# Optimization experiments

Measured on AMD Instinct MI355X. Metric: run time of the kernel, lower is better.

The kernel has to match this reference:

```python
import jax, jax.numpy as jnp
import numpy as np

NUM_HEADS = 8
POS_DIM = 4
LEFT_CTX = 512


def setup_inputs() -> dict:
    key = jax.random.key(0)
    ks = jax.random.split(key, 9)
    S, B, E, A, H, P, L = 512, 16, 512, 512, NUM_HEADS, POS_DIM, LEFT_CTX
    in_out = 2 * A + A // 2 + H * P  # 1312
    S2 = 2 * S - 1 + L  # 1535
    return {
        "x": jax.random.normal(ks[0], (S, B, E), jnp.float32) * 0.1,
        "cached_key": jax.random.normal(ks[1], (L, B, A), jnp.float32) * 0.1,
        "cached_val": jax.random.normal(ks[2], (L, B, A // 2), jnp.float32) * 0.1,
        "pos_emb": jax.random.normal(ks[3], (1, S2, E), jnp.float32) * 0.1,
        "in_proj_w": jax.random.normal(ks[4], (in_out, E), jnp.float32) * 0.02,
        "in_proj_b": jnp.zeros((in_out,), jnp.float32),
        "linear_pos_w": jax.random.normal(ks[5], (H * P, E), jnp.float32) * 0.02,
        "out_proj_w": jax.random.normal(ks[6], (E, A // 2), jnp.float32) * 0.02,
        "out_proj_b": jnp.zeros((E,), jnp.float32),
    }


def reference(x, cached_key, cached_val, pos_emb, in_proj_w, in_proj_b,
              linear_pos_w, out_proj_w, out_proj_b):
    S, B, E = x.shape
    L = cached_key.shape[0]
    A = cached_key.shape[-1]          # attention_dim
    H, P = NUM_HEADS, POS_DIM
    hd = A // H                        # head_dim
    vd = hd // 2                       # value head dim

    # in_proj (nn.Linear): (S, B, 2A + A/2 + H*P)
    xp = jnp.einsum('sbe,oe->sbo', x, in_proj_w) + in_proj_b
    q = xp[..., :A]
    k_new = xp[..., A:2 * A]
    v_new = xp[..., 2 * A:2 * A + A // 2]
    p = xp[..., 2 * A + A // 2:]

    # pad+add == concat(cached, new) along time
    k = jnp.concatenate([cached_key, k_new], axis=0)   # (kv, B, A)
    v = jnp.concatenate([cached_val, v_new], axis=0)   # (kv, B, A/2)
    cached_key_out = k[-L:]
    cached_val_out = v[-L:]
    kv = k.shape[0]

    q4 = q.reshape(S, B, H, hd)
    p4 = p.reshape(S, B, H, P)
    k4 = k.reshape(kv, B, H, hd)
    v4 = v.reshape(kv, B, H, vd)

    # relative position bias: linear_pos has no bias
    S2 = pos_emb.shape[1]              # 2S - 1 + L
    pos = (jnp.einsum('one,pe->onp', pos_emb, linear_pos_w)
           .reshape(S2, H, P))          # (S2, H, P)
    pos_weights = jnp.einsum('sbhp,nhp->bhsn', p4, pos)  # (B, H, S, S2)

    # as_strided relative shift: out[b,h,t,j] = pw[b,h,t, (S-1) - t + j]
    idx = (S - 1) - jnp.arange(S)[:, None] + jnp.arange(kv)[None, :]  # (S, kv)
    pos_weights = jnp.take_along_axis(pos_weights, idx[None, None], axis=3)

    scores = jnp.einsum('sbhd,nbhd->bhsn', q4, k4) + pos_weights  # (B,H,S,kv)
    attn = jax.nn.softmax(scores, axis=-1)

    out = jnp.einsum('bhsn,nbhd->sbhd', attn, v4).reshape(S, B, A // 2)
    out = jnp.einsum('sbd,ed->sbe', out, out_proj_w) + out_proj_b

    weights = attn.reshape(B * H, S, kv)
    return out, weights, cached_key_out, cached_val_out
```

## Files before the change

### kernel.cpp

```cpp
#include <hip/hip_runtime.h>
#include <math.h>


using f32x4  = __attribute__((ext_vector_type(4))) float;
using bf16x8 = __attribute__((ext_vector_type(8))) short;

__device__ __forceinline__ unsigned short f2bf(float f) {
    unsigned u = __builtin_bit_cast(unsigned, f);
    u = (u + 0x7FFFu + ((u >> 16) & 1u)) >> 16;
    return (unsigned short)u;
}
__device__ __forceinline__ float bf2f(unsigned short s) {
    return __builtin_bit_cast(float, (unsigned)s << 16);
}

__device__ __forceinline__ void cvt8(const float* __restrict__ src,
                                     unsigned short* __restrict__ dst, int i)
{
    float4 v0 = *(const float4*)(src + i);
    float4 v1 = *(const float4*)(src + i + 4);
    unsigned short tmp[8] = { f2bf(v0.x), f2bf(v0.y), f2bf(v0.z), f2bf(v0.w),
                              f2bf(v1.x), f2bf(v1.y), f2bf(v1.z), f2bf(v1.w) };
    *(int4*)(dst + i) = *(const int4*)tmp;
}

__global__ __launch_bounds__(256)
void prep(const float* __restrict__ x, const float* __restrict__ in_proj_w,
          const float* __restrict__ out_proj_w, const float* __restrict__ ck_in,
          const float* __restrict__ pos_emb, const float* __restrict__ lpw,
          unsigned short* __restrict__ xb, unsigned short* __restrict__ wb,
          unsigned short* __restrict__ opw, unsigned short* __restrict__ kb,
          float* __restrict__ pos_ws)
{
    __shared__ float As[16][68];
    __shared__ float Bs[16][68];
    const int bid = blockIdx.x, t = threadIdx.x;
    if (bid < 2048) {
        cvt8(x, xb, (bid * 256 + t) * 8);
    } else if (bid < 2376) {
        cvt8(in_proj_w, wb, ((bid - 2048) * 256 + t) * 8);
    } else if (bid < 2440) {
        cvt8(out_proj_w, opw, ((bid - 2376) * 256 + t) * 8);
    } else if (bid < 3464) {
        const int i  = bid - 2440;
        const int n0 = (i & 63) * 8;
        const int b  = i >> 6;
        const int c  = t * 2;
        const int h  = c >> 6, d = c & 63;
        #pragma unroll
        for (int j = 0; j < 8; ++j) {
            const int n = n0 + j;
            float2 v = *(const float2*)(ck_in + ((size_t)n * 16 + b) * 512 + c);
            unsigned short tmp[2] = { f2bf(v.x), f2bf(v.y) };
            *(unsigned int*)(kb + (((size_t)b*8 + h)*1024 + n)*64 + d)
                = *(const unsigned int*)tmp;
        }
    } else {
        const int m0 = (bid - 3464) * 64;
        const int lr = t >> 2, lc = (t & 3) * 4;
        const int tx = t & 15, ty = t >> 4;
        float acc[4][4] = {};
        for (int k0 = 0; k0 < 512; k0 += 16) {
            float4 av = make_float4(0.f,0.f,0.f,0.f);
            float4 bv = make_float4(0.f,0.f,0.f,0.f);
            if (m0 + lr < 1535) av = *(const float4*)(pos_emb + (size_t)(m0 + lr) * 512 + k0 + lc);
            if (lr < 32)        bv = *(const float4*)(lpw + (size_t)lr * 512 + k0 + lc);
            __syncthreads();
            As[lc+0][lr] = av.x; As[lc+1][lr] = av.y; As[lc+2][lr] = av.z; As[lc+3][lr] = av.w;
            Bs[lc+0][lr] = bv.x; Bs[lc+1][lr] = bv.y; Bs[lc+2][lr] = bv.z; Bs[lc+3][lr] = bv.w;
            __syncthreads();
            #pragma unroll
            for (int kk = 0; kk < 16; ++kk) {
                float4 a4 = *(const float4*)&As[kk][ty * 4];
                float4 b4 = *(const float4*)&Bs[kk][tx * 4];
                float af[4] = {a4.x, a4.y, a4.z, a4.w};
                float bf[4] = {b4.x, b4.y, b4.z, b4.w};
                #pragma unroll
                for (int i2 = 0; i2 < 4; ++i2)
                    #pragma unroll
                    for (int j = 0; j < 4; ++j)
                        acc[i2][j] += af[i2] * bf[j];
            }
        }
        const int n = tx * 4;
        if (n < 32) {
            #pragma unroll
            for (int i2 = 0; i2 < 4; ++i2) {
                const int mi = m0 + ty * 4 + i2;
                if (mi >= 1535) break;
                #pragma unroll
                for (int j = 0; j < 4; ++j)
                    pos_ws[(size_t)mi * 32 + n + j] = acc[i2][j];
            }
        }
    }
}

__global__ __launch_bounds__(256)
void mfma_gemm_nt(const unsigned short* __restrict__ A,
                  const unsigned short* __restrict__ B,
                  const float* __restrict__ bias, int K, int N, int NBLK, int mode,
                  float* __restrict__ C, int ldc,
                  unsigned short* __restrict__ qb, float* __restrict__ ck,
                  unsigned short* __restrict__ kb, float* __restrict__ cv,
                  float* __restrict__ p_ws)
{
    __shared__ unsigned short smem[6144];
    const int t  = threadIdx.x;
    const int wv = t >> 6, l = t & 63;
    const int lr = l & 15, g = l >> 4;
    const int bid = blockIdx.x;
    const int xcd = bid & 7, i = bid >> 3;
    const int my  = xcd + 8 * (i / NBLK);
    const int nx  = i % NBLK;
    const int m0b = my * 128;
    const int m0  = m0b + wv * 32;
    const int n0  = nx * 64;

    const int srow = t >> 2, soct = t & 3;
    const unsigned short* Ag0 = A + (size_t)(m0b + srow) * K + soct * 8;
    const unsigned short* Ag1 = Ag0 + (size_t)64 * K;
    const unsigned short* Bg  = B + (size_t)(n0 + srow) * K + soct * 8;
    const int oa0 = (soct * 128 + srow) * 8;
    const int oa1 = oa0 + 64 * 8;
    const int ob  = 4096 + (soct * 64 + srow) * 8;

    const int ra0 = (g * 128 + wv * 32 + lr) * 8;
    const int ra1 = ra0 + 16 * 8;
    const int rb  = 4096 + (g * 64 + lr) * 8;

    f32x4 acc[2][4] = {};

    bf16x8 sa0 = *(const bf16x8*)(Ag0);
    bf16x8 sa1 = *(const bf16x8*)(Ag1);
    bf16x8 sb  = *(const bf16x8*)(Bg);

    const int NK = K >> 5;
    for (int t16 = 0; t16 < NK; ++t16) {
        __syncthreads();
        *(bf16x8*)(smem + oa0) = sa0;
        *(bf16x8*)(smem + oa1) = sa1;
        *(bf16x8*)(smem + ob)  = sb;
        __syncthreads();
        if (t16 + 1 < NK) {
            const int k0 = (t16 + 1) * 32;
            sa0 = *(const bf16x8*)(Ag0 + k0);
            sa1 = *(const bf16x8*)(Ag1 + k0);
            sb  = *(const bf16x8*)(Bg + k0);
        }
        bf16x8 a0 = *(const bf16x8*)(smem + ra0);
        bf16x8 a1 = *(const bf16x8*)(smem + ra1);
        bf16x8 b0 = *(const bf16x8*)(smem + rb);
        bf16x8 b1 = *(const bf16x8*)(smem + rb + 16 * 8);
        bf16x8 b2 = *(const bf16x8*)(smem + rb + 32 * 8);
        bf16x8 b3 = *(const bf16x8*)(smem + rb + 48 * 8);
        acc[0][0] = __builtin_amdgcn_mfma_f32_16x16x32_bf16(a0, b0, acc[0][0], 0, 0, 0);
        acc[0][1] = __builtin_amdgcn_mfma_f32_16x16x32_bf16(a0, b1, acc[0][1], 0, 0, 0);
        acc[0][2] = __builtin_amdgcn_mfma_f32_16x16x32_bf16(a0, b2, acc[0][2], 0, 0, 0);
        acc[0][3] = __builtin_amdgcn_mfma_f32_16x16x32_bf16(a0, b3, acc[0][3], 0, 0, 0);
        acc[1][0] = __builtin_amdgcn_mfma_f32_16x16x32_bf16(a1, b0, acc[1][0], 0, 0, 0);
        acc[1][1] = __builtin_amdgcn_mfma_f32_16x16x32_bf16(a1, b1, acc[1][1], 0, 0, 0);
        acc[1][2] = __builtin_amdgcn_mfma_f32_16x16x32_bf16(a1, b2, acc[1][2], 0, 0, 0);
        acc[1][3] = __builtin_amdgcn_mfma_f32_16x16x32_bf16(a1, b3, acc[1][3], 0, 0, 0);
    }

    const int rbase = g * 4;
    const int nf = (N - n0) >= 64 ? 4 : (N - n0) >> 4;
    #pragma unroll
    for (int fi = 0; fi < 2; ++fi) {
        for (int fj = 0; fj < nf; ++fj) {
            const f32x4& a = acc[fi][fj];
            const int c = n0 + fj * 16 + lr;
            const float bs = bias ? bias[c] : 0.f;
            #pragma unroll
            for (int r = 0; r < 4; ++r) {
                const int m = m0 + fi * 16 + rbase + r;
                const float v = a[r] + bs;
                if (mode == 0) {
                    C[(size_t)m * ldc + c] = v;
                } else {
                    const int s = m >> 4, bb = m & 15;
                    if (c < 512) {
                        const int hh = c >> 6, dd = c & 63;
                        qb[(((size_t)bb*8 + hh)*512 + s)*64 + dd] = f2bf(v);
                    } else if (c < 1024) {
                        const int cc = c - 512;
                        __builtin_nontemporal_store(v, ck + (size_t)m * 512 + cc);
                        const int hh = cc >> 6, dd = cc & 63;
                        kb[(((size_t)bb*8 + hh)*1024 + 512 + s)*64 + dd] = f2bf(v);
                    } else if (c < 1280) {
                        cv[(size_t)m * 256 + (c - 1024)] = v;
                    } else {
                        p_ws[(size_t)m * 32 + (c - 1280)] = v;
                    }
                }
            }
        }
    }
}

__global__ __launch_bounds__(256)
void transpose_v(const float* __restrict__ cv_in, const float* __restrict__ cv_new,
                 unsigned short* __restrict__ vt)
{
    const int t  = threadIdx.x;
    const int n0 = blockIdx.x * 128;
    const int bh = blockIdx.y;
    const int b  = bh >> 3, h = bh & 7;

    __shared__ float tile[128][33];

    #pragma unroll
    for (int k = 0; k < 4; ++k) {
        const int nl = (t >> 3) + k * 32;
        const int n  = n0 + nl;
        const int c4 = (t & 7) * 4;
        const float* src = (n < 512)
            ? cv_in  + ((size_t)n * 16 + b) * 256 + h * 32 + c4
            : cv_new + ((size_t)(n - 512) * 16 + b) * 256 + h * 32 + c4;
        float4 v = *(const float4*)src;
        tile[nl][c4 + 0] = v.x; tile[nl][c4 + 1] = v.y;
        tile[nl][c4 + 2] = v.z; tile[nl][c4 + 3] = v.w;
    }
    __syncthreads();
    {
        const int d  = t >> 3;
        const int nb = (t & 7) * 16;
        unsigned short tmp[16];
        #pragma unroll
        for (int j = 0; j < 16; ++j) tmp[j] = f2bf(tile[nb + j][d]);
        unsigned short* dst = vt + ((size_t)bh * 32 + d) * 1024 + n0 + nb;
        *(int4*)(dst)     = *(const int4*)(tmp);
        *(int4*)(dst + 8) = *(const int4*)(tmp + 8);
    }
}

__global__ __launch_bounds__(256, 4)
void attn_fused2(const unsigned short* __restrict__ qb,
                 const float* __restrict__ p_ws,
                 const float* __restrict__ pos_ws,
                 const unsigned short* __restrict__ kb,
                 const unsigned short* __restrict__ vt,
                 float* __restrict__ weights,
                 unsigned short* __restrict__ ao)
{
    const int t  = threadIdx.x;
    const int wv = t >> 6, l = t & 63;
    const int lr = l & 15, ks0 = (l >> 4) * 8, rbase = (l >> 4) * 4;
    const int idx = blockIdx.x;
    const int kq  = idx >> 3;
    const int bh  = (idx & 7) + 8 * (kq >> 5);
    const int s0  = (kq & 31) * 16;
    const int b   = bh >> 3, h = bh & 7;

    union SM { float4 pos[1039]; unsigned short e[16][1064]; };
    __shared__ SM u;
    __shared__ float pvred[4][16][16];
    __shared__ float red_l[4][16];

    const int j0 = 496 - s0;
    for (int j = t; j < 1039; j += 256)
        u.pos[j] = *(const float4*)(pos_ws + (size_t)(j0 + j) * 32 + h * 4);

    const unsigned short* qp = qb + ((size_t)bh * 512 + s0 + lr) * 64 + ks0;
    bf16x8 qa0 = *(const bf16x8*)(qp);
    bf16x8 qa1 = *(const bf16x8*)(qp + 32);

    float4 p4r[4];
    #pragma unroll
    for (int r = 0; r < 4; ++r)
        p4r[r] = *(const float4*)(p_ws + ((size_t)(s0 + rbase + r) * 16 + b) * 32 + h * 4);

    const unsigned short* kbase = kb + ((size_t)bh * 1024 + wv * 256) * 64;
    f32x4 sc[16];
    #pragma unroll
    for (int i = 0; i < 16; ++i) sc[i] = (f32x4){0.f,0.f,0.f,0.f};

    #pragma unroll
    for (int tile = 0; tile < 16; ++tile) {
        const unsigned short* kp = kbase + (size_t)(tile * 16 + lr) * 64 + ks0;
        bf16x8 k0 = *(const bf16x8*)(kp);
        bf16x8 k1 = *(const bf16x8*)(kp + 32);
        sc[tile] = __builtin_amdgcn_mfma_f32_16x16x32_bf16(qa0, k0, sc[tile], 0, 0, 0);
        sc[tile] = __builtin_amdgcn_mfma_f32_16x16x32_bf16(qa1, k1, sc[tile], 0, 0, 0);
    }

    __syncthreads();

    float sm[4] = {0.f, 0.f, 0.f, 0.f};
    #pragma unroll
    for (int tile = 0; tile < 16; ++tile) {
        const int nidx = wv * 256 + tile * 16 + lr;
        #pragma unroll
        for (int r = 0; r < 4; ++r) {
            float4 pp = u.pos[15 - rbase - r + nidx];
            float e = __expf(sc[tile][r] + p4r[r].x * pp.x + p4r[r].y * pp.y
                                         + p4r[r].z * pp.z + p4r[r].w * pp.w);
            sc[tile][r] = e;
            sm[r] += e;
        }
    }
    #pragma unroll
    for (int r = 0; r < 4; ++r) {
        #pragma unroll
        for (int off = 1; off < 16; off <<= 1) sm[r] += __shfl_xor(sm[r], off);
    }

    __syncthreads();

    if (lr == 0) {
        #pragma unroll
        for (int r = 0; r < 4; ++r) red_l[wv][rbase + r] = sm[r];
    }
    #pragma unroll
    for (int tile = 0; tile < 16; ++tile) {
        const int nidx = wv * 256 + tile * 16 + lr;
        #pragma unroll
        for (int r = 0; r < 4; ++r)
            u.e[rbase + r][nidx] = f2bf(sc[tile][r]);
    }
    __syncthreads();

    const int kh = wv >> 1, dt = wv & 1;
    f32x4 paA = {0.f, 0.f, 0.f, 0.f}, paB = {0.f, 0.f, 0.f, 0.f};
    const unsigned short* vrow = vt + ((size_t)bh * 32 + dt * 16 + lr) * 1024;
    #pragma unroll
    for (int kstep = 0; kstep < 8; ++kstep) {
        const int kk = kh * 512 + kstep * 32 + ks0;
        bf16x8 wa = *(const bf16x8*)&u.e[lr][kk];
        bf16x8 vb = *(const bf16x8*)(vrow + kk);
        paA = __builtin_amdgcn_mfma_f32_16x16x32_bf16(wa, vb, paA, 0, 0, 0);
    }
    #pragma unroll
    for (int kstep = 8; kstep < 16; ++kstep) {
        const int kk = kh * 512 + kstep * 32 + ks0;
        bf16x8 wa = *(const bf16x8*)&u.e[lr][kk];
        bf16x8 vb = *(const bf16x8*)(vrow + kk);
        paB = __builtin_amdgcn_mfma_f32_16x16x32_bf16(wa, vb, paB, 0, 0, 0);
    }

    const size_t wb_base = ((size_t)bh * 512 + s0) * 1024;
    #pragma unroll
    for (int i2 = 0; i2 < 8; ++i2) {
        const int id2 = t + i2 * 256;
        const int r   = id2 >> 7;
        const int c8  = (id2 & 127) * 8;
        const float il = 1.0f / (red_l[0][r] + red_l[1][r] + red_l[2][r] + red_l[3][r]);
        bf16x8 ev = *(const bf16x8*)&u.e[r][c8];
        f32x4 o0, o1;
        o0[0] = bf2f((unsigned short)ev[0]) * il;
        o0[1] = bf2f((unsigned short)ev[1]) * il;
        o0[2] = bf2f((unsigned short)ev[2]) * il;
        o0[3] = bf2f((unsigned short)ev[3]) * il;
        o1[0] = bf2f((unsigned short)ev[4]) * il;
        o1[1] = bf2f((unsigned short)ev[5]) * il;
        o1[2] = bf2f((unsigned short)ev[6]) * il;
        o1[3] = bf2f((unsigned short)ev[7]) * il;
        __builtin_nontemporal_store(o0, (f32x4*)(weights + wb_base + (size_t)r * 1024 + c8));
        __builtin_nontemporal_store(o1, (f32x4*)(weights + wb_base + (size_t)r * 1024 + c8 + 4));
    }

    #pragma unroll
    for (int r = 0; r < 4; ++r)
        pvred[wv][rbase + r][lr] = paA[r] + paB[r];
    __syncthreads();
    #pragma unroll
    for (int i3 = 0; i3 < 2; ++i3) {
        const int id3 = t + i3 * 256;
        const int r = id3 >> 5, d = id3 & 31;
        const int dt2 = d >> 4, dl = d & 15;
        const float il = 1.0f / (red_l[0][r] + red_l[1][r] + red_l[2][r] + red_l[3][r]);
        float v = (pvred[dt2][r][dl] + pvred[2 + dt2][r][dl]) * il;
        ao[((size_t)(s0 + r) * 16 + b) * 256 + h * 32 + d] = f2bf(v);
    }
}

extern "C" void kernel_launch(void* const* d_in, const int* in_sizes, int n_in,
                              void* d_out, int out_size, void* d_ws, size_t ws_size,
                              hipStream_t stream)
{
    const float* x            = (const float*)d_in[0];
    const float* cached_key   = (const float*)d_in[1];
    const float* cached_val   = (const float*)d_in[2];
    const float* pos_emb      = (const float*)d_in[3];
    const float* in_proj_w    = (const float*)d_in[4];
    const float* in_proj_b    = (const float*)d_in[5];
    const float* linear_pos_w = (const float*)d_in[6];
    const float* out_proj_w   = (const float*)d_in[7];
    const float* out_proj_b   = (const float*)d_in[8];

    float* out     = (float*)d_out;
    float* weights = out + 4194304;
    float* ck_new  = weights + 67108864;
    float* cv_new  = ck_new + 4194304;

    float* ws      = (float*)d_ws;
    float* p_ws    = ws;
    float* pos_ws  = ws + 262144;
    unsigned short* ao_b  = (unsigned short*)(ws + 311264);
    unsigned short* opw_b = (unsigned short*)(ws + 1359840);
    unsigned short* qb    = (unsigned short*)(ws + 1425376);
    unsigned short* kb    = (unsigned short*)(ws + 3522528);
    unsigned short* vt    = (unsigned short*)(ws + 7716832);
    unsigned short* xb    = (unsigned short*)(ws + 9813984);
    unsigned short* wb    = (unsigned short*)(ws + 11911136);

    prep<<<3488, 256, 0, stream>>>(x, in_proj_w, out_proj_w, cached_key,
                                   pos_emb, linear_pos_w,
                                   xb, wb, opw_b, kb, pos_ws);
    mfma_gemm_nt<<<1344, 256, 0, stream>>>(xb, wb, in_proj_b, 512, 1312, 21, 1,
                                           nullptr, 0,
                                           qb, ck_new, kb, cv_new, p_ws);
    transpose_v<<<dim3(8, 128), 256, 0, stream>>>(cached_val, cv_new, vt);
    attn_fused2<<<4096, 256, 0, stream>>>(qb, p_ws, pos_ws, kb, vt,
                                          weights, ao_b);
    mfma_gemm_nt<<<512, 256, 0, stream>>>(ao_b, opw_b, out_proj_b, 256, 512, 8, 0,
                                          out, 512,
                                          nullptr, nullptr, nullptr, nullptr,
                                          nullptr);
}
```

Before: 214.7 us.

## Fuse V transpose into prep and GEMM epilogue, double GEMM K-step

Removes the standalone transpose_v kernel. The cached-value half of the transpose moves into new prep blocks, and the GEMM epilogue now writes the new V values directly in transposed bf16 layout. The GEMM main loop now stages 64 K-elements per barrier pair instead of 32, which doubles shared memory use but halves the number of synchronizations. It also moves the p_ws loads in attention after the QK MFMA loop. The intent is to save one launch plus a global round trip, at the cost of scattered 2-byte stores in the epilogue.

Measured after the change: 229.7 us. 1.07x slower.

```diff
diff --git a/kernel.cpp b/kernel.cpp
--- a/kernel.cpp
+++ b/kernel.cpp
@@ -28,12 +28,16 @@
 void prep(const float* __restrict__ x, const float* __restrict__ in_proj_w,
           const float* __restrict__ out_proj_w, const float* __restrict__ ck_in,
           const float* __restrict__ pos_emb, const float* __restrict__ lpw,
+          const float* __restrict__ cv_in,
           unsigned short* __restrict__ xb, unsigned short* __restrict__ wb,
           unsigned short* __restrict__ opw, unsigned short* __restrict__ kb,
-          float* __restrict__ pos_ws)
+          float* __restrict__ pos_ws, unsigned short* __restrict__ vt)
 {
-    __shared__ float As[16][68];
-    __shared__ float Bs[16][68];
+    union SH {
+        struct { float As[16][68]; float Bs[16][68]; } g;
+        float tile[128][33];
+    };
+    __shared__ SH sh;
     const int bid = blockIdx.x, t = threadIdx.x;
     if (bid < 2048) {
         cvt8(x, xb, (bid * 256 + t) * 8);
@@ -55,7 +59,7 @@
             *(unsigned int*)(kb + (((size_t)b*8 + h)*1024 + n)*64 + d)
                 = *(const unsigned int*)tmp;
         }
-    } else {
+    } else if (bid < 3488) {
         const int m0 = (bid - 3464) * 64;
         const int lr = t >> 2, lc = (t & 3) * 4;
         const int tx = t & 15, ty = t >> 4;
@@ -66,13 +70,15 @@
             if (m0 + lr < 1535) av = *(const float4*)(pos_emb + (size_t)(m0 + lr) * 512 + k0 + lc);
             if (lr < 32)        bv = *(const float4*)(lpw + (size_t)lr * 512 + k0 + lc);
             __syncthreads();
-            As[lc+0][lr] = av.x; As[lc+1][lr] = av.y; As[lc+2][lr] = av.z; As[lc+3][lr] = av.w;
-            Bs[lc+0][lr] = bv.x; Bs[lc+1][lr] = bv.y; Bs[lc+2][lr] = bv.z; Bs[lc+3][lr] = bv.w;
+            sh.g.As[lc+0][lr] = av.x; sh.g.As[lc+1][lr] = av.y;
+            sh.g.As[lc+2][lr] = av.z; sh.g.As[lc+3][lr] = av.w;
+            sh.g.Bs[lc+0][lr] = bv.x; sh.g.Bs[lc+1][lr] = bv.y;
+            sh.g.Bs[lc+2][lr] = bv.z; sh.g.Bs[lc+3][lr] = bv.w;
             __syncthreads();
             #pragma unroll
             for (int kk = 0; kk < 16; ++kk) {
-                float4 a4 = *(const float4*)&As[kk][ty * 4];
-                float4 b4 = *(const float4*)&Bs[kk][tx * 4];
+                float4 a4 = *(const float4*)&sh.g.As[kk][ty * 4];
+                float4 b4 = *(const float4*)&sh.g.Bs[kk][tx * 4];
                 float af[4] = {a4.x, a4.y, a4.z, a4.w};
                 float bf[4] = {b4.x, b4.y, b4.z, b4.w};
                 #pragma unroll
@@ -93,6 +99,31 @@
                     pos_ws[(size_t)mi * 32 + n + j] = acc[i2][j];
             }
         }
+    } else {
+        const int i  = bid - 3488;
+        const int n0 = (i & 3) * 128;
+        const int bh = i >> 2;
+        const int b  = bh >> 3, h = bh & 7;
+        #pragma unroll
+        for (int k = 0; k < 4; ++k) {
+            const int nl = (t >> 3) + k * 32;
+            const int c4 = (t & 7) * 4;
+            float4 v = *(const float4*)(cv_in
+                + ((size_t)(n0 + nl) * 16 + b) * 256 + h * 32 + c4);
+            sh.tile[nl][c4 + 0] = v.x; sh.tile[nl][c4 + 1] = v.y;
+            sh.tile[nl][c4 + 2] = v.z; sh.tile[nl][c4 + 3] = v.w;
+        }
+        __syncthreads();
+        {
+            const int d  = t >> 3;
+            const int nb = (t & 7) * 16;
+            unsigned short tmp[16];
+            #pragma unroll
+            for (int j = 0; j < 16; ++j) tmp[j] = f2bf(sh.tile[nb + j][d]);
+            unsigned short* dst = vt + ((size_t)bh * 32 + d) * 1024 + n0 + nb;
+            *(int4*)(dst)     = *(const int4*)(tmp);
+            *(int4*)(dst + 8) = *(const int4*)(tmp + 8);
+        }
     }
 }
 
@@ -103,9 +134,9 @@
                   float* __restrict__ C, int ldc,
                   unsigned short* __restrict__ qb, float* __restrict__ ck,
                   unsigned short* __restrict__ kb, float* __restrict__ cv,
-                  float* __restrict__ p_ws)
+                  float* __restrict__ p_ws, unsigned short* __restrict__ vt)
 {
-    __shared__ unsigned short smem[6144];
+    __shared__ unsigned short smem[12288];
     const int t  = threadIdx.x;
     const int wv = t >> 6, l = t & 63;
     const int lr = l & 15, g = l >> 4;
@@ -123,45 +154,58 @@
     const unsigned short* Bg  = B + (size_t)(n0 + srow) * K + soct * 8;
     const int oa0 = (soct * 128 + srow) * 8;
     const int oa1 = oa0 + 64 * 8;
-    const int ob  = 4096 + (soct * 64 + srow) * 8;
+    const int ob  = 8192 + (soct * 64 + srow) * 8;
 
     const int ra0 = (g * 128 + wv * 32 + lr) * 8;
     const int ra1 = ra0 + 16 * 8;
-    const int rb  = 4096 + (g * 64 + lr) * 8;
+    const int rb  = 8192 + (g * 64 + lr) * 8;
 
     f32x4 acc[2][4] = {};
 
-    bf16x8 sa0 = *(const bf16x8*)(Ag0);
-    bf16x8 sa1 = *(const bf16x8*)(Ag1);
-    bf16x8 sb  = *(const bf16x8*)(Bg);
-
-    const int NK = K >> 5;
-    for (int t16 = 0; t16 < NK; ++t16) {
+    bf16x8 sa0h0 = *(const bf16x8*)(Ag0);
+    bf16x8 sa0h1 = *(const bf16x8*)(Ag0 + 32);
+    bf16x8 sa1h0 = *(const bf16x8*)(Ag1);
+    bf16x8 sa1h1 = *(const bf16x8*)(Ag1 + 32);
+    bf16x8 sbh0  = *(const bf16x8*)(Bg);
+    bf16x8 sbh1  = *(const bf16x8*)(Bg + 32);
+
+    const int NK = K >> 6;
+    for (int it = 0; it < NK; ++it) {
         __syncthreads();
-        *(bf16x8*)(smem + oa0) = sa0;
-        *(bf16x8*)(smem + oa1) = sa1;
-        *(bf16x8*)(smem + ob)  = sb;
+        *(bf16x8*)(smem + oa0)        = sa0h0;
+        *(bf16x8*)(smem + 4096 + oa0) = sa0h1;
+        *(bf16x8*)(smem + oa1)        = sa1h0;
+        *(bf16x8*)(smem + 4096 + oa1) = sa1h1;
+        *(bf16x8*)(smem + ob)         = sbh0;
+        *(bf16x8*)(smem + 2048 + ob)  = sbh1;
         __syncthreads();
-        if (t16 + 1 < NK) {
-            const int k0 = (t16 + 1) * 32;
-            sa0 = *(const bf16x8*)(Ag0 + k0);
-            sa1 = *(const bf16x8*)(Ag1 + k0);
-            sb  = *(const bf16x8*)(Bg + k0);
-        }
-        bf16x8 a0 = *(const bf16x8*)(smem + ra0);
-        bf16x8 a1 = *(const bf16x8*)(smem + ra1);
-        bf16x8 b0 = *(const bf16x8*)(smem + rb);
-        bf16x8 b1 = *(const bf16x8*)(smem + rb + 16 * 8);
-        bf16x8 b2 = *(const bf16x8*)(smem + rb + 32 * 8);
-        bf16x8 b3 = *(const bf16x8*)(smem + rb + 48 * 8);
-        acc[0][0] = __builtin_amdgcn_mfma_f32_16x16x32_bf16(a0, b0, acc[0][0], 0, 0, 0);
-        acc[0][1] = __builtin_amdgcn_mfma_f32_16x16x32_bf16(a0, b1, acc[0][1], 0, 0, 0);
-        acc[0][2] = __builtin_amdgcn_mfma_f32_16x16x32_bf16(a0, b2, acc[0][2], 0, 0, 0);
-        acc[0][3] = __builtin_amdgcn_mfma_f32_16x16x32_bf16(a0, b3, acc[0][3], 0, 0, 0);
-        acc[1][0] = __builtin_amdgcn_mfma_f32_16x16x32_bf16(a1, b0, acc[1][0], 0, 0, 0);
-        acc[1][1] = __builtin_amdgcn_mfma_f32_16x16x32_bf16(a1, b1, acc[1][1], 0, 0, 0);
-        acc[1][2] = __builtin_amdgcn_mfma_f32_16x16x32_bf16(a1, b2, acc[1][2], 0, 0, 0);
-        acc[1][3] = __builtin_amdgcn_mfma_f32_16x16x32_bf16(a1, b3, acc[1][3], 0, 0, 0);
+        if (it + 1 < NK) {
+            const int k0 = (it + 1) * 64;
+            sa0h0 = *(const bf16x8*)(Ag0 + k0);
+            sa0h1 = *(const bf16x8*)(Ag0 + k0 + 32);
+            sa1h0 = *(const bf16x8*)(Ag1 + k0);
+            sa1h1 = *(const bf16x8*)(Ag1 + k0 + 32);
+            sbh0  = *(const bf16x8*)(Bg + k0);
+            sbh1  = *(const bf16x8*)(Bg + k0 + 32);
+        }
+        #pragma unroll
+        for (int h = 0; h < 2; ++h) {
+            const int ab = h * 4096, bb2 = h * 2048;
+            bf16x8 a0 = *(const bf16x8*)(smem + ab + ra0);
+            bf16x8 a1 = *(const bf16x8*)(smem + ab + ra1);
+            bf16x8 b0 = *(const bf16x8*)(smem + bb2 + rb);
+            bf16x8 b1 = *(const bf16x8*)(smem + bb2 + rb + 16 * 8);
+            bf16x8 b2 = *(const bf16x8*)(smem + bb2 + rb + 32 * 8);
+            bf16x8 b3 = *(const bf16x8*)(smem + bb2 + rb + 48 * 8);
+            acc[0][0] = __builtin_amdgcn_mfma_f32_16x16x32_bf16(a0, b0, acc[0][0], 0, 0, 0);
+            acc[0][1] = __builtin_amdgcn_mfma_f32_16x16x32_bf16(a0, b1, acc[0][1], 0, 0, 0);
+            acc[0][2] = __builtin_amdgcn_mfma_f32_16x16x32_bf16(a0, b2, acc[0][2], 0, 0, 0);
+            acc[0][3] = __builtin_amdgcn_mfma_f32_16x16x32_bf16(a0, b3, acc[0][3], 0, 0, 0);
+            acc[1][0] = __builtin_amdgcn_mfma_f32_16x16x32_bf16(a1, b0, acc[1][0], 0, 0, 0);
+            acc[1][1] = __builtin_amdgcn_mfma_f32_16x16x32_bf16(a1, b1, acc[1][1], 0, 0, 0);
+            acc[1][2] = __builtin_amdgcn_mfma_f32_16x16x32_bf16(a1, b2, acc[1][2], 0, 0, 0);
+            acc[1][3] = __builtin_amdgcn_mfma_f32_16x16x32_bf16(a1, b3, acc[1][3], 0, 0, 0);
+        }
     }
 
     const int rbase = g * 4;
@@ -189,49 +233,16 @@
                         const int hh = cc >> 6, dd = cc & 63;
                         kb[(((size_t)bb*8 + hh)*1024 + 512 + s)*64 + dd] = f2bf(v);
                     } else if (c < 1280) {
-                        cv[(size_t)m * 256 + (c - 1024)] = v;
+                        const int cc = c - 1024;
+                        cv[(size_t)m * 256 + cc] = v;
+                        const int hh = cc >> 5, dd = cc & 31;
+                        vt[(((size_t)bb*8 + hh)*32 + dd)*1024 + 512 + s] = f2bf(v);
                     } else {
                         p_ws[(size_t)m * 32 + (c - 1280)] = v;
                     }
                 }
             }
         }
-    }
-}
-
-__global__ __launch_bounds__(256)
-void transpose_v(const float* __restrict__ cv_in, const float* __restrict__ cv_new,
-                 unsigned short* __restrict__ vt)
-{
-    const int t  = threadIdx.x;
-    const int n0 = blockIdx.x * 128;
-    const int bh = blockIdx.y;
-    const int b  = bh >> 3, h = bh & 7;
-
-    __shared__ float tile[128][33];
-
-    #pragma unroll
-    for (int k = 0; k < 4; ++k) {
-        const int nl = (t >> 3) + k * 32;
-        const int n  = n0 + nl;
-        const int c4 = (t & 7) * 4;
-        const float* src = (n < 512)
-            ? cv_in  + ((size_t)n * 16 + b) * 256 + h * 32 + c4
-            : cv_new + ((size_t)(n - 512) * 16 + b) * 256 + h * 32 + c4;
-        float4 v = *(const float4*)src;
-        tile[nl][c4 + 0] = v.x; tile[nl][c4 + 1] = v.y;
-        tile[nl][c4 + 2] = v.z; tile[nl][c4 + 3] = v.w;
-    }
-    __syncthreads();
-    {
-        const int d  = t >> 3;
-        const int nb = (t & 7) * 16;
-        unsigned short tmp[16];
-        #pragma unroll
-        for (int j = 0; j < 16; ++j) tmp[j] = f2bf(tile[nb + j][d]);
-        unsigned short* dst = vt + ((size_t)bh * 32 + d) * 1024 + n0 + nb;
-        *(int4*)(dst)     = *(const int4*)(tmp);
-        *(int4*)(dst + 8) = *(const int4*)(tmp + 8);
     }
 }
 
@@ -266,11 +277,6 @@
     bf16x8 qa0 = *(const bf16x8*)(qp);
     bf16x8 qa1 = *(const bf16x8*)(qp + 32);
 
-    float4 p4r[4];
-    #pragma unroll
-    for (int r = 0; r < 4; ++r)
-        p4r[r] = *(const float4*)(p_ws + ((size_t)(s0 + rbase + r) * 16 + b) * 32 + h * 4);
-
     const unsigned short* kbase = kb + ((size_t)bh * 1024 + wv * 256) * 64;
     f32x4 sc[16];
     #pragma unroll
@@ -284,6 +290,11 @@
         sc[tile] = __builtin_amdgcn_mfma_f32_16x16x32_bf16(qa0, k0, sc[tile], 0, 0, 0);
         sc[tile] = __builtin_amdgcn_mfma_f32_16x16x32_bf16(qa1, k1, sc[tile], 0, 0, 0);
     }
+
+    float4 p4r[4];
+    #pragma unroll
+    for (int r = 0; r < 4; ++r)
+        p4r[r] = *(const float4*)(p_ws + ((size_t)(s0 + rbase + r) * 16 + b) * 32 + h * 4);
 
     __syncthreads();
 
@@ -405,17 +416,16 @@
     unsigned short* xb    = (unsigned short*)(ws + 9813984);
     unsigned short* wb    = (unsigned short*)(ws + 11911136);
 
-    prep<<<3488, 256, 0, stream>>>(x, in_proj_w, out_proj_w, cached_key,
-                                   pos_emb, linear_pos_w,
-                                   xb, wb, opw_b, kb, pos_ws);
+    prep<<<4000, 256, 0, stream>>>(x, in_proj_w, out_proj_w, cached_key,
+                                   pos_emb, linear_pos_w, cached_val,
+                                   xb, wb, opw_b, kb, pos_ws, vt);
     mfma_gemm_nt<<<1344, 256, 0, stream>>>(xb, wb, in_proj_b, 512, 1312, 21, 1,
                                            nullptr, 0,
-                                           qb, ck_new, kb, cv_new, p_ws);
-    transpose_v<<<dim3(8, 128), 256, 0, stream>>>(cached_val, cv_new, vt);
+                                           qb, ck_new, kb, cv_new, p_ws, vt);
     attn_fused2<<<4096, 256, 0, stream>>>(qb, p_ws, pos_ws, kb, vt,
                                           weights, ao_b);
     mfma_gemm_nt<<<512, 256, 0, stream>>>(ao_b, opw_b, out_proj_b, 256, 512, 8, 0,
                                           out, 512,
                                           nullptr, nullptr, nullptr, nullptr,
-                                          nullptr);
-}
+                                          nullptr, nullptr);
+}
```
